# Kernel tuning notes

Measured on AMD Instinct MI355X. Metric: run time of the kernel, lower is better.

The kernel has to match this reference:

```python
import jax, jax.numpy as jnp
import numpy as np
import math

E = 4096  # embed_dim
H = 32    # num_heads
M = 256   # max_queries
B = 8     # batch
N = 256   # kv tokens (16x16 grid -> no pos-embed interpolation branch)


def _sincos_1d(d, pos):
    omega = np.arange(d // 2, dtype=np.float32) / (d / 2.0)
    omega = 1.0 / 10000 ** omega
    out = np.einsum('m,d->md', pos.reshape(-1), omega)
    return np.concatenate([np.sin(out), np.cos(out)], axis=1)


def _sincos_2d(embed_dim, grid_size):
    gh = np.arange(grid_size, dtype=np.float32)
    gw = np.arange(grid_size, dtype=np.float32)
    grid = np.stack(np.meshgrid(gw, gh), axis=0).reshape(2, -1)
    return np.concatenate([
        _sincos_1d(embed_dim // 2, grid[0]),
        _sincos_1d(embed_dim // 2, grid[1]),
    ], axis=1)


def setup_inputs() -> dict:
    key = jax.random.key(0)
    ks = jax.random.split(key, 4)
    grid_size = int(math.ceil(math.sqrt(M)))
    pe = _sincos_2d(E, grid_size)[:M].astype(np.float32)
    return {
        'x': jax.random.normal(ks[0], (B, N, E), jnp.float32),
        'query': 0.02 * jax.random.normal(ks[1], (M, E), jnp.float32),
        'pos_embed': jnp.asarray(pe),
        'ln_q_w': jnp.ones((E,), jnp.float32),
        'ln_q_b': jnp.zeros((E,), jnp.float32),
        'ln_kv_w': jnp.ones((E,), jnp.float32),
        'ln_kv_b': jnp.zeros((E,), jnp.float32),
        'in_proj_w': 0.02 * jax.random.normal(ks[2], (3 * E, E), jnp.float32),
        'in_proj_b': jnp.zeros((3 * E,), jnp.float32),
        'out_proj_w': 0.02 * jax.random.normal(ks[3], (E, E), jnp.float32),
        'out_proj_b': jnp.zeros((E,), jnp.float32),
    }


def _ln(x, w, b, eps=1e-5):
    m = jnp.mean(x, -1, keepdims=True)
    v = jnp.mean((x - m) ** 2, -1, keepdims=True)
    return (x - m) * jax.lax.rsqrt(v + eps) * w + b


def reference(x, query, pos_embed, ln_q_w, ln_q_b, ln_kv_w, ln_kv_b,
              in_proj_w, in_proj_b, out_proj_w, out_proj_b):
    D = E // H
    kv = _ln(x, ln_kv_w, ln_kv_b)                      # [B,N,E] (kv_proj is Identity)
    q_in = _ln(query, ln_q_w, ln_q_b) + pos_embed      # [M,E] (Q + posQ, shared over batch)
    k_in = kv + pos_embed[None]                        # N == M so posK == pos_embed (no interp)
    Wq, Wk, Wv = in_proj_w[:E], in_proj_w[E:2 * E], in_proj_w[2 * E:]
    bq, bk, bv = in_proj_b[:E], in_proj_b[E:2 * E], in_proj_b[2 * E:]
    q = (q_in @ Wq.T + bq).reshape(M, H, D).transpose(1, 0, 2)          # [H,M,D]
    k = (k_in @ Wk.T + bk).reshape(B, N, H, D).transpose(0, 2, 1, 3)    # [B,H,N,D]
    v = (kv @ Wv.T + bv).reshape(B, N, H, D).transpose(0, 2, 1, 3)      # [B,H,N,D]
    scores = jnp.einsum('hmd,bhnd->bhmn', q, k) / jnp.sqrt(jnp.float32(D))
    attn = jax.nn.softmax(scores, axis=-1)                              # [B,H,M,N]
    o = jnp.einsum('bhmn,bhnd->bhmd', attn, v)
    o = o.transpose(0, 2, 1, 3).reshape(B, M, E)
    out = o @ out_proj_w.T + out_proj_b                                 # [B,M,E]
    # need_weights=True with average_attn_weights=True -> head-averaged weights
    return out, attn.mean(axis=1)
```

## Files before the change

### kernel.cpp

```cpp
#include <hip/hip_runtime.h>
#include <hip/hip_bf16.h>

typedef __bf16 bf16;
typedef __attribute__((ext_vector_type(8))) __bf16 bf16x8;
typedef __attribute__((ext_vector_type(4))) __bf16 bf16x4;
typedef __attribute__((ext_vector_type(4))) float floatx4;

#define E_DIM 4096
#define H_DIM 32
#define D_DIM 128
#define M_DIM 256
#define B_DIM 8
#define N_DIM 256

#define GLD_LDS(g, l) __builtin_amdgcn_global_load_lds( \
    (const __attribute__((address_space(1))) unsigned int*)(g), \
    (__attribute__((address_space(3))) unsigned int*)(l), 16, 0, 0)

__device__ __forceinline__ float wave_sum(float v) {
#pragma unroll
  for (int o = 32; o; o >>= 1) v += __shfl_xor(v, o);
  return v;
}
__device__ __forceinline__ float wave_max(float v) {
#pragma unroll
  for (int o = 32; o; o >>= 1) v = fmaxf(v, __shfl_xor(v, o));
  return v;
}

__global__ __launch_bounds__(256) void cvt_kernel(const float* __restrict__ src,
                                                  bf16* __restrict__ dst, long n) {
  long i = ((long)blockIdx.x * 256 + threadIdx.x) * 8;
  if (i >= n) return;
  float4 a = *(const float4*)(src + i);
  float4 b = *(const float4*)(src + i + 4);
  bf16x8 p;
  p[0] = (bf16)a.x; p[1] = (bf16)a.y; p[2] = (bf16)a.z; p[3] = (bf16)a.w;
  p[4] = (bf16)b.x; p[5] = (bf16)b.y; p[6] = (bf16)b.z; p[7] = (bf16)b.w;
  *(bf16x8*)(dst + i) = p;
}

__global__ __launch_bounds__(256) void ln_x_kernel(const float* __restrict__ x,
                                                   const float* __restrict__ w,
                                                   const float* __restrict__ bvec,
                                                   const float* __restrict__ pos,
                                                   bf16* __restrict__ kv,
                                                   bf16* __restrict__ kin) {
  const int row = blockIdx.x;
  const int n = row & (N_DIM - 1);
  const int tid = threadIdx.x, wid = tid >> 6, lane = tid & 63;
  const float* xr = x + (size_t)row * E_DIM;
  float4 v[4];
  float s1 = 0.f, s2 = 0.f;
#pragma unroll
  for (int j = 0; j < 4; ++j) {
    v[j] = *(const float4*)(xr + j * 1024 + tid * 4);
    s1 += v[j].x + v[j].y + v[j].z + v[j].w;
    s2 += v[j].x * v[j].x + v[j].y * v[j].y + v[j].z * v[j].z + v[j].w * v[j].w;
  }
  s1 = wave_sum(s1); s2 = wave_sum(s2);
  __shared__ float red[8];
  if (lane == 0) { red[wid] = s1; red[wid + 4] = s2; }
  __syncthreads();
  s1 = red[0] + red[1] + red[2] + red[3];
  s2 = red[4] + red[5] + red[6] + red[7];
  const float mean = s1 * (1.f / E_DIM);
  const float var = s2 * (1.f / E_DIM) - mean * mean;
  const float rs = rsqrtf(var + 1e-5f);
#pragma unroll
  for (int j = 0; j < 4; ++j) {
    const int idx = j * 1024 + tid * 4;
    float4 wv = *(const float4*)(w + idx);
    float4 bv = *(const float4*)(bvec + idx);
    float4 pv = *(const float4*)(pos + (size_t)n * E_DIM + idx);
    float y0 = (v[j].x - mean) * rs * wv.x + bv.x;
    float y1 = (v[j].y - mean) * rs * wv.y + bv.y;
    float y2 = (v[j].z - mean) * rs * wv.z + bv.z;
    float y3 = (v[j].w - mean) * rs * wv.w + bv.w;
    bf16x4 a; a[0] = (bf16)y0; a[1] = (bf16)y1; a[2] = (bf16)y2; a[3] = (bf16)y3;
    *(bf16x4*)(kv + (size_t)row * E_DIM + idx) = a;
    bf16x4 c; c[0] = (bf16)(y0 + pv.x); c[1] = (bf16)(y1 + pv.y);
    c[2] = (bf16)(y2 + pv.z); c[3] = (bf16)(y3 + pv.w);
    *(bf16x4*)(kin + (size_t)row * E_DIM + idx) = c;
  }
}

__global__ __launch_bounds__(256) void ln_q_kernel(const float* __restrict__ q,
                                                   const float* __restrict__ w,
                                                   const float* __restrict__ bvec,
                                                   const float* __restrict__ pos,
                                                   bf16* __restrict__ qin) {
  const int row = blockIdx.x;
  const int tid = threadIdx.x, wid = tid >> 6, lane = tid & 63;
  const float* xr = q + (size_t)row * E_DIM;
  float4 v[4];
  float s1 = 0.f, s2 = 0.f;
#pragma unroll
  for (int j = 0; j < 4; ++j) {
    v[j] = *(const float4*)(xr + j * 1024 + tid * 4);
    s1 += v[j].x + v[j].y + v[j].z + v[j].w;
    s2 += v[j].x * v[j].x + v[j].y * v[j].y + v[j].z * v[j].z + v[j].w * v[j].w;
  }
  s1 = wave_sum(s1); s2 = wave_sum(s2);
  __shared__ float red[8];
  if (lane == 0) { red[wid] = s1; red[wid + 4] = s2; }
  __syncthreads();
  s1 = red[0] + red[1] + red[2] + red[3];
  s2 = red[4] + red[5] + red[6] + red[7];
  const float mean = s1 * (1.f / E_DIM);
  const float var = s2 * (1.f / E_DIM) - mean * mean;
  const float rs = rsqrtf(var + 1e-5f);
#pragma unroll
  for (int j = 0; j < 4; ++j) {
    const int idx = j * 1024 + tid * 4;
    float4 wv = *(const float4*)(w + idx);
    float4 bv = *(const float4*)(bvec + idx);
    float4 pv = *(const float4*)(pos + (size_t)row * E_DIM + idx);
    bf16x4 a;
    a[0] = (bf16)((v[j].x - mean) * rs * wv.x + bv.x + pv.x);
    a[1] = (bf16)((v[j].y - mean) * rs * wv.y + bv.y + pv.y);
    a[2] = (bf16)((v[j].z - mean) * rs * wv.z + bv.z + pv.z);
    a[3] = (bf16)((v[j].w - mean) * rs * wv.w + bv.w + pv.w);
    *(bf16x4*)(qin + (size_t)row * E_DIM + idx) = a;
  }
}

template <int MODE>
__global__ __launch_bounds__(256, 2)
void gemm_bt(const bf16* __restrict__ Abase, const bf16* __restrict__ Bbase,
             const float* __restrict__ bias, float* __restrict__ Cf,
             bf16* __restrict__ Cb, int M, int N, int K, int lda, int ldb, int ldc,
             float scale) {
  __shared__ __align__(16) bf16 As[4096];
  __shared__ __align__(16) bf16 Bs[4096];
  const int tid = threadIdx.x;
  const int wid = tid >> 6;
  const int lane = tid & 63;

  const bf16* A = Abase;
  const bf16* B = Bbase;
  int zb = 0, zh = 0;
  if constexpr (MODE == 2) {
    int z = blockIdx.z; zb = z >> 5; zh = z & 31;
    A += zh * D_DIM;
    B += ((size_t)zb * N_DIM) * E_DIM + zh * D_DIM;
  } else if constexpr (MODE == 3) {
    int z = blockIdx.z; zb = z >> 5; zh = z & 31;
    A += (size_t)z * M_DIM * 512;
    B += (size_t)z * D_DIM * N_DIM;
  }

  const bf16* Arow = A + (size_t)(blockIdx.y * 128) * lda;
  const bf16* Brow = B + (size_t)(blockIdx.x * 128) * ldb;

  const int s0 = wid * 2;
  const int srow = lane >> 2;
  const int skoff = (lane & 3) * 8;

  floatx4 acc[4][4];
#pragma unroll
  for (int i = 0; i < 4; ++i)
#pragma unroll
    for (int j = 0; j < 4; ++j) acc[i][j] = (floatx4){0.f, 0.f, 0.f, 0.f};

  const int rA = (wid >> 1) * 64 + (lane & 15);
  const int rB = (wid & 1) * 64 + (lane & 15);
  const int q16 = (lane >> 4) * 8;

  const int kTiles = K >> 5;
  for (int kt = 0; kt < kTiles; ++kt) {
    const int k0 = kt << 5;
#pragma unroll
    for (int c = 0; c < 2; ++c) {
      const int s = s0 + c;
      const int row = s * 16 + srow;
      GLD_LDS(Arow + (size_t)row * lda + k0 + skoff, As + s * 512);
      GLD_LDS(Brow + (size_t)row * ldb + k0 + skoff, Bs + s * 512);
    }
    asm volatile("s_waitcnt vmcnt(0)" ::: "memory");
    __syncthreads();

    bf16x8 af[4], bfr[4];
#pragma unroll
    for (int t = 0; t < 4; ++t) {
      af[t] = *(const bf16x8*)(As + (rA + t * 16) * 32 + q16);
      bfr[t] = *(const bf16x8*)(Bs + (rB + t * 16) * 32 + q16);
    }
#pragma unroll
    for (int tr = 0; tr < 4; ++tr)
#pragma unroll
      for (int tc = 0; tc < 4; ++tc)
        acc[tr][tc] = __builtin_amdgcn_mfma_f32_16x16x32_bf16(af[tr], bfr[tc],
                                                              acc[tr][tc], 0, 0, 0);
    __syncthreads();
  }

  const int mb = blockIdx.y * 128 + (wid >> 1) * 64 + (lane >> 4) * 4;
  const int nb = blockIdx.x * 128 + (wid & 1) * 64 + (lane & 15);
#pragma unroll
  for (int tr = 0; tr < 4; ++tr) {
#pragma unroll
    for (int tc = 0; tc < 4; ++tc) {
      const int row0 = mb + tr * 16;
      const int col = nb + tc * 16;
      floatx4 a = acc[tr][tc];
      if constexpr (MODE == 0) {
        const float bb = bias[col];
#pragma unroll
        for (int r = 0; r < 4; ++r)
          Cb[(size_t)(row0 + r) * ldc + col] = (bf16)(a[0 + r] + bb);
      } else if constexpr (MODE == 1) {
        const float bb = bias[col];
        const int h = col >> 7, d = col & 127;
        const int b_ = row0 >> 8, n_ = row0 & 255;
        bf16x4 p;
#pragma unroll
        for (int r = 0; r < 4; ++r) p[r] = (bf16)(a[r] + bb);
        *(bf16x4*)(Cb + ((size_t)((b_ * H_DIM + h) * D_DIM + d)) * N_DIM + n_) = p;
      } else if constexpr (MODE == 2) {
#pragma unroll
        for (int r = 0; r < 4; ++r)
          Cf[(size_t)blockIdx.z * (M_DIM * N_DIM) + (size_t)(row0 + r) * ldc + col] =
              a[r] * scale;
      } else if constexpr (MODE == 3) {
#pragma unroll
        for (int r = 0; r < 4; ++r)
          Cb[(size_t)zb * M_DIM * E_DIM + (size_t)(row0 + r) * E_DIM + zh * D_DIM + col] =
              (bf16)a[r];
      } else {
        const float bb = bias[col];
#pragma unroll
        for (int r = 0; r < 4; ++r)
          Cf[(size_t)(row0 + r) * ldc + col] = a[r] + bb;
      }
    }
  }
}

__global__ __launch_bounds__(256) void softmax_mean_kernel(float* __restrict__ scores,
                                                           float* __restrict__ out_mean) {
  const int bm = blockIdx.x;
  const int b = bm >> 8, m = bm & 255;
  const int wid = threadIdx.x >> 6, lane = threadIdx.x & 63;
  float a0 = 0.f, a1 = 0.f, a2 = 0.f, a3 = 0.f;
  for (int j = 0; j < 8; ++j) {
    const int h = wid * 8 + j;
    float* row = scores + ((size_t)((b * H_DIM + h) * M_DIM + m)) * N_DIM;
    float4 v = *(const float4*)(row + lane * 4);
    float mx = fmaxf(fmaxf(v.x, v.y), fmaxf(v.z, v.w));
    mx = wave_max(mx);
    v.x = __expf(v.x - mx); v.y = __expf(v.y - mx);
    v.z = __expf(v.z - mx); v.w = __expf(v.w - mx);
    const float s = wave_sum(v.x + v.y + v.z + v.w);
    const float inv = 1.f / s;
    v.x *= inv; v.y *= inv; v.z *= inv; v.w *= inv;
    a0 += v.x; a1 += v.y; a2 += v.z; a3 += v.w;
    bf16x4 p; p[0] = (bf16)v.x; p[1] = (bf16)v.y; p[2] = (bf16)v.z; p[3] = (bf16)v.w;
    *(bf16x4*)((bf16*)row + lane * 4) = p;
  }
  __shared__ float red[4][256];
  *(float4*)&red[wid][lane * 4] = make_float4(a0, a1, a2, a3);
  __syncthreads();
  if (wid == 0) {
    float4 r0 = *(float4*)&red[0][lane * 4];
    float4 r1 = *(float4*)&red[1][lane * 4];
    float4 r2 = *(float4*)&red[2][lane * 4];
    float4 r3 = *(float4*)&red[3][lane * 4];
    float4 o;
    o.x = (r0.x + r1.x + r2.x + r3.x) * (1.f / H_DIM);
    o.y = (r0.y + r1.y + r2.y + r3.y) * (1.f / H_DIM);
    o.z = (r0.z + r1.z + r2.z + r3.z) * (1.f / H_DIM);
    o.w = (r0.w + r1.w + r2.w + r3.w) * (1.f / H_DIM);
    *(float4*)(out_mean + (size_t)bm * N_DIM + lane * 4) = o;
  }
}

extern "C" void kernel_launch(void* const* d_in, const int* in_sizes, int n_in,
                              void* d_out, int out_size, void* d_ws, size_t ws_size,
                              hipStream_t stream) {
  const float* x = (const float*)d_in[0];
  const float* query = (const float*)d_in[1];
  const float* pos = (const float*)d_in[2];
  const float* ln_q_w = (const float*)d_in[3];
  const float* ln_q_b = (const float*)d_in[4];
  const float* ln_kv_w = (const float*)d_in[5];
  const float* ln_kv_b = (const float*)d_in[6];
  const float* Wqkv_f = (const float*)d_in[7];
  const float* bqkv = (const float*)d_in[8];
  const float* Wout_f = (const float*)d_in[9];
  const float* bout = (const float*)d_in[10];

  char* ws = (char*)d_ws;
  bf16* Wqkv = (bf16*)(ws + 0);
  bf16* Wout = (bf16*)(ws + 100663296);
  bf16* kv   = (bf16*)(ws + 134217728);
  bf16* kin  = (bf16*)(ws + 150994944);
  bf16* qin  = (bf16*)(ws + 167772160);
  bf16* qp   = (bf16*)(ws + 169869312);
  bf16* kp   = (bf16*)(ws + 171966464);
  bf16* vt   = (bf16*)(ws + 188743680);
  float* scores = (float*)(ws + 0);
  bf16* obuf = (bf16*)(ws + 67108864);

  float* out = (float*)d_out;
  float* out2 = out + (size_t)B_DIM * M_DIM * E_DIM;

  cvt_kernel<<<24576, 256, 0, stream>>>(Wqkv_f, Wqkv, 50331648L);
  cvt_kernel<<<8192, 256, 0, stream>>>(Wout_f, Wout, 16777216L);
  ln_x_kernel<<<2048, 256, 0, stream>>>(x, ln_kv_w, ln_kv_b, pos, kv, kin);
  ln_q_kernel<<<256, 256, 0, stream>>>(query, ln_q_w, ln_q_b, pos, qin);

  gemm_bt<0><<<dim3(32, 2, 1), 256, 0, stream>>>(qin, Wqkv, bqkv, nullptr, qp,
                                                 256, 4096, 4096, 4096, 4096, 4096, 1.f);
  gemm_bt<0><<<dim3(32, 16, 1), 256, 0, stream>>>(kin, Wqkv + (size_t)4096 * 4096,
                                                  bqkv + 4096, nullptr, kp,
                                                  2048, 4096, 4096, 4096, 4096, 4096, 1.f);
  gemm_bt<1><<<dim3(32, 16, 1), 256, 0, stream>>>(kv, Wqkv + (size_t)2 * 4096 * 4096,
                                                  bqkv + 8192, nullptr, vt,
                                                  2048, 4096, 4096, 4096, 4096, 4096, 1.f);
  gemm_bt<2><<<dim3(2, 2, 256), 256, 0, stream>>>(qp, kp, nullptr, scores, nullptr,
                                                  256, 256, 128, 4096, 4096, 256,
                                                  0.08838834764831845f);
  softmax_mean_kernel<<<2048, 256, 0, stream>>>(scores, out2);
  gemm_bt<3><<<dim3(1, 2, 256), 256, 0, stream>>>((const bf16*)scores, vt, nullptr,
                                                  nullptr, obuf,
                                                  256, 128, 256, 512, 256, 4096, 1.f);
  gemm_bt<4><<<dim3(32, 16, 1), 256, 0, stream>>>(obuf, Wout, bout, out, nullptr,
                                                  2048, 4096, 4096, 4096, 4096, 4096, 1.f);
}
```

Before: 850.1 us.

## Fuse QKV projections into one launch and split-K the output projection

Merges the two weight-conversion kernels into one launch and the three Q/K/V projection GEMMs into one grouped kernel with 1088 blocks, so the small Q GEMM no longer runs as its own underfilled launch. The output projection is split along K into two halves written to fp32 partial buffers, followed by a reduce kernel that adds the partials and the bias. This raises the out-proj grid to 1024 blocks to better fill the CUs. Launch bounds go from 2 to 4 blocks per CU, which limits registers per thread and could cause spills in the 4x4 MFMA accumulator tile. The split-K path also adds extra fp32 traffic for the partials.

After: 789.5 us. 7.1% less time.

```diff
diff --git a/kernel.cpp b/kernel.cpp
--- a/kernel.cpp
+++ b/kernel.cpp
@@ -28,16 +28,21 @@
   return v;
 }
 
-__global__ __launch_bounds__(256) void cvt_kernel(const float* __restrict__ src,
-                                                  bf16* __restrict__ dst, long n) {
+__global__ __launch_bounds__(256) void cvt_all_kernel(const float* __restrict__ s1,
+                                                      bf16* __restrict__ d1,
+                                                      const float* __restrict__ s2,
+                                                      bf16* __restrict__ d2) {
   long i = ((long)blockIdx.x * 256 + threadIdx.x) * 8;
-  if (i >= n) return;
-  float4 a = *(const float4*)(src + i);
-  float4 b = *(const float4*)(src + i + 4);
+  const float* src;
+  bf16* dst;
+  if (i < 50331648L) { src = s1 + i; dst = d1 + i; }
+  else { src = s2 + (i - 50331648L); dst = d2 + (i - 50331648L); }
+  float4 a = *(const float4*)(src);
+  float4 b = *(const float4*)(src + 4);
   bf16x8 p;
   p[0] = (bf16)a.x; p[1] = (bf16)a.y; p[2] = (bf16)a.z; p[3] = (bf16)a.w;
   p[4] = (bf16)b.x; p[5] = (bf16)b.y; p[6] = (bf16)b.z; p[7] = (bf16)b.w;
-  *(bf16x8*)(dst + i) = p;
+  *(bf16x8*)(dst) = p;
 }
 
 __global__ __launch_bounds__(256) void ln_x_kernel(const float* __restrict__ x,
@@ -125,12 +130,108 @@
   }
 }
 
+__global__ __launch_bounds__(256, 4)
+void proj_fused(const bf16* __restrict__ qin, const bf16* __restrict__ kin,
+                const bf16* __restrict__ kv, const bf16* __restrict__ Wqkv,
+                const float* __restrict__ bqkv, bf16* __restrict__ qp,
+                bf16* __restrict__ kp, bf16* __restrict__ vt) {
+  __shared__ __align__(16) bf16 As[4096];
+  __shared__ __align__(16) bf16 Bs[4096];
+  const int tid = threadIdx.x;
+  const int wid = tid >> 6;
+  const int lane = tid & 63;
+
+  const int id = blockIdx.x;
+  int role, bx, by;
+  const bf16 *A, *B;
+  const float* bias;
+  bf16* C;
+  if (id < 512) {
+    role = 1; bx = id & 31; by = id >> 5;
+    A = kin; B = Wqkv + 16777216; bias = bqkv + 4096; C = kp;
+  } else if (id < 1024) {
+    role = 2; bx = (id - 512) & 31; by = (id - 512) >> 5;
+    A = kv; B = Wqkv + 33554432; bias = bqkv + 8192; C = vt;
+  } else {
+    role = 0; bx = (id - 1024) & 31; by = (id - 1024) >> 5;
+    A = qin; B = Wqkv; bias = bqkv; C = qp;
+  }
+
+  const bf16* Arow = A + (size_t)(by * 128) * E_DIM;
+  const bf16* Brow = B + (size_t)(bx * 128) * E_DIM;
+
+  const int s0 = wid * 2;
+  const int srow = lane >> 2;
+  const int skoff = (lane & 3) * 8;
+
+  floatx4 acc[4][4];
+#pragma unroll
+  for (int i = 0; i < 4; ++i)
+#pragma unroll
+    for (int j = 0; j < 4; ++j) acc[i][j] = (floatx4){0.f, 0.f, 0.f, 0.f};
+
+  const int rA = (wid >> 1) * 64 + (lane & 15);
+  const int rB = (wid & 1) * 64 + (lane & 15);
+  const int q16 = (lane >> 4) * 8;
+
+  for (int kt = 0; kt < 128; ++kt) {
+    const int k0 = kt << 5;
+#pragma unroll
+    for (int c = 0; c < 2; ++c) {
+      const int s = s0 + c;
+      const int row = s * 16 + srow;
+      GLD_LDS(Arow + (size_t)row * E_DIM + k0 + skoff, As + s * 512);
+      GLD_LDS(Brow + (size_t)row * E_DIM + k0 + skoff, Bs + s * 512);
+    }
+    asm volatile("s_waitcnt vmcnt(0)" ::: "memory");
+    __syncthreads();
+
+    bf16x8 af[4], bfr[4];
+#pragma unroll
+    for (int t = 0; t < 4; ++t) {
+      af[t] = *(const bf16x8*)(As + (rA + t * 16) * 32 + q16);
+      bfr[t] = *(const bf16x8*)(Bs + (rB + t * 16) * 32 + q16);
+    }
+#pragma unroll
+    for (int tr = 0; tr < 4; ++tr)
+#pragma unroll
+      for (int tc = 0; tc < 4; ++tc)
+        acc[tr][tc] = __builtin_amdgcn_mfma_f32_16x16x32_bf16(af[tr], bfr[tc],
+                                                              acc[tr][tc], 0, 0, 0);
+    __syncthreads();
+  }
+
+  const int mb = by * 128 + (wid >> 1) * 64 + (lane >> 4) * 4;
+  const int nb = bx * 128 + (wid & 1) * 64 + (lane & 15);
+#pragma unroll
+  for (int tr = 0; tr < 4; ++tr) {
+#pragma unroll
+    for (int tc = 0; tc < 4; ++tc) {
+      const int row0 = mb + tr * 16;
+      const int col = nb + tc * 16;
+      const float bb = bias[col];
+      floatx4 a = acc[tr][tc];
+      if (role != 2) {
+#pragma unroll
+        for (int r = 0; r < 4; ++r)
+          C[(size_t)(row0 + r) * E_DIM + col] = (bf16)(a[r] + bb);
+      } else {
+        const int h = col >> 7, d = col & 127;
+        const int b_ = row0 >> 8, n_ = row0 & 255;
+        bf16x4 p;
+#pragma unroll
+        for (int r = 0; r < 4; ++r) p[r] = (bf16)(a[r] + bb);
+        *(bf16x4*)(C + ((size_t)((b_ * H_DIM + h) * D_DIM + d)) * N_DIM + n_) = p;
+      }
+    }
+  }
+}
+
 template <int MODE>
-__global__ __launch_bounds__(256, 2)
+__global__ __launch_bounds__(256, 4)
 void gemm_bt(const bf16* __restrict__ Abase, const bf16* __restrict__ Bbase,
-             const float* __restrict__ bias, float* __restrict__ Cf,
-             bf16* __restrict__ Cb, int M, int N, int K, int lda, int ldb, int ldc,
-             float scale) {
+             float* __restrict__ Cf, bf16* __restrict__ Cb,
+             int K, int lda, int ldb, int ldc, float scale) {
   __shared__ __align__(16) bf16 As[4096];
   __shared__ __align__(16) bf16 Bs[4096];
   const int tid = threadIdx.x;
@@ -148,6 +249,9 @@
     int z = blockIdx.z; zb = z >> 5; zh = z & 31;
     A += (size_t)z * M_DIM * 512;
     B += (size_t)z * D_DIM * N_DIM;
+  } else if constexpr (MODE == 5) {
+    A += blockIdx.z * 2048;
+    B += blockIdx.z * 2048;
   }
 
   const bf16* Arow = A + (size_t)(blockIdx.y * 128) * lda;
@@ -204,37 +308,37 @@
       const int row0 = mb + tr * 16;
       const int col = nb + tc * 16;
       floatx4 a = acc[tr][tc];
-      if constexpr (MODE == 0) {
-        const float bb = bias[col];
-#pragma unroll
-        for (int r = 0; r < 4; ++r)
-          Cb[(size_t)(row0 + r) * ldc + col] = (bf16)(a[0 + r] + bb);
-      } else if constexpr (MODE == 1) {
-        const float bb = bias[col];
-        const int h = col >> 7, d = col & 127;
-        const int b_ = row0 >> 8, n_ = row0 & 255;
-        bf16x4 p;
-#pragma unroll
-        for (int r = 0; r < 4; ++r) p[r] = (bf16)(a[r] + bb);
-        *(bf16x4*)(Cb + ((size_t)((b_ * H_DIM + h) * D_DIM + d)) * N_DIM + n_) = p;
-      } else if constexpr (MODE == 2) {
+      if constexpr (MODE == 2) {
 #pragma unroll
         for (int r = 0; r < 4; ++r)
           Cf[(size_t)blockIdx.z * (M_DIM * N_DIM) + (size_t)(row0 + r) * ldc + col] =
               a[r] * scale;
       } else if constexpr (MODE == 3) {
+        int z = blockIdx.z; int zb_ = z >> 5, zh_ = z & 31;
 #pragma unroll
         for (int r = 0; r < 4; ++r)
-          Cb[(size_t)zb * M_DIM * E_DIM + (size_t)(row0 + r) * E_DIM + zh * D_DIM + col] =
+          Cb[(size_t)zb_ * M_DIM * E_DIM + (size_t)(row0 + r) * E_DIM + zh_ * D_DIM + col] =
               (bf16)a[r];
       } else {
-        const float bb = bias[col];
 #pragma unroll
         for (int r = 0; r < 4; ++r)
-          Cf[(size_t)(row0 + r) * ldc + col] = a[r] + bb;
+          Cf[(size_t)blockIdx.z * 8388608 + (size_t)(row0 + r) * ldc + col] = a[r];
       }
     }
   }
+}
+
+__global__ __launch_bounds__(256) void reduce_out_kernel(const float* __restrict__ p,
+                                                         const float* __restrict__ bias,
+                                                         float* __restrict__ out) {
+  const size_t i = ((size_t)blockIdx.x * 256 + threadIdx.x) * 4;
+  float4 a = *(const float4*)(p + i);
+  float4 b = *(const float4*)(p + 8388608 + i);
+  float4 bb = *(const float4*)(bias + (i & 4095));
+  float4 o;
+  o.x = a.x + b.x + bb.x; o.y = a.y + b.y + bb.y;
+  o.z = a.z + b.z + bb.z; o.w = a.w + b.w + bb.w;
+  *(float4*)(out + i) = o;
 }
 
 __global__ __launch_bounds__(256) void softmax_mean_kernel(float* __restrict__ scores,
@@ -299,32 +403,27 @@
   bf16* qp   = (bf16*)(ws + 169869312);
   bf16* kp   = (bf16*)(ws + 171966464);
   bf16* vt   = (bf16*)(ws + 188743680);
+  float* partials = (float*)(ws + 205520896);
   float* scores = (float*)(ws + 0);
   bf16* obuf = (bf16*)(ws + 67108864);
 
   float* out = (float*)d_out;
   float* out2 = out + (size_t)B_DIM * M_DIM * E_DIM;
 
-  cvt_kernel<<<24576, 256, 0, stream>>>(Wqkv_f, Wqkv, 50331648L);
-  cvt_kernel<<<8192, 256, 0, stream>>>(Wout_f, Wout, 16777216L);
+  cvt_all_kernel<<<32768, 256, 0, stream>>>(Wqkv_f, Wqkv, Wout_f, Wout);
   ln_x_kernel<<<2048, 256, 0, stream>>>(x, ln_kv_w, ln_kv_b, pos, kv, kin);
   ln_q_kernel<<<256, 256, 0, stream>>>(query, ln_q_w, ln_q_b, pos, qin);
 
-  gemm_bt<0><<<dim3(32, 2, 1), 256, 0, stream>>>(qin, Wqkv, bqkv, nullptr, qp,
-                                                 256, 4096, 4096, 4096, 4096, 4096, 1.f);
-  gemm_bt<0><<<dim3(32, 16, 1), 256, 0, stream>>>(kin, Wqkv + (size_t)4096 * 4096,
-                                                  bqkv + 4096, nullptr, kp,
-                                                  2048, 4096, 4096, 4096, 4096, 4096, 1.f);
-  gemm_bt<1><<<dim3(32, 16, 1), 256, 0, stream>>>(kv, Wqkv + (size_t)2 * 4096 * 4096,
-                                                  bqkv + 8192, nullptr, vt,
-                                                  2048, 4096, 4096, 4096, 4096, 4096, 1.f);
-  gemm_bt<2><<<dim3(2, 2, 256), 256, 0, stream>>>(qp, kp, nullptr, scores, nullptr,
-                                                  256, 256, 128, 4096, 4096, 256,
+  proj_fused<<<1088, 256, 0, stream>>>(qin, kin, kv, Wqkv, bqkv, qp, kp, vt);
+
+  gemm_bt<2><<<dim3(2, 2, 256), 256, 0, stream>>>(qp, kp, scores, nullptr,
+                                                  128, 4096, 4096, 256,
                                                   0.08838834764831845f);
   softmax_mean_kernel<<<2048, 256, 0, stream>>>(scores, out2);
-  gemm_bt<3><<<dim3(1, 2, 256), 256, 0, stream>>>((const bf16*)scores, vt, nullptr,
+  gemm_bt<3><<<dim3(1, 2, 256), 256, 0, stream>>>((const bf16*)scores, vt,
                                                   nullptr, obuf,
-                                                  256, 128, 256, 512, 256, 4096, 1.f);
-  gemm_bt<4><<<dim3(32, 16, 1), 256, 0, stream>>>(obuf, Wout, bout, out, nullptr,
-                                                  2048, 4096, 4096, 4096, 4096, 4096, 1.f);
-}
+                                                  256, 512, 256, 4096, 1.f);
+  gemm_bt<5><<<dim3(32, 16, 2), 256, 0, stream>>>(obuf, Wout, partials, nullptr,
+                                                  2048, 4096, 4096, 4096, 1.f);
+  reduce_out_kernel<<<8192, 256, 0, stream>>>(partials, bout, out);
+}
```
